# Optimization experiments

Measured on AMD Instinct MI355X. Metric: run time of the kernel, lower is better.

Reference implementation:

```python
import jax, jax.numpy as jnp
import numpy as np

D = 1024      # model_size
H = 16        # n_heads
HD = D // H   # head_size
B = 8
S = 1024


def setup_inputs() -> dict:
    key = jax.random.key(0)
    ks = jax.random.split(key, 8)
    sq = lambda k, shp: jax.random.normal(k, shp, dtype=jnp.float32) * (1.0 / np.sqrt(shp[0]))
    return {
        "query": jax.random.normal(ks[0], (B, S, D), dtype=jnp.float32),
        "value": jax.random.normal(ks[1], (B, S, D), dtype=jnp.float32),
        "Wq": sq(ks[2], (D, D)),
        "bq": jnp.zeros((D,), dtype=jnp.float32),
        "Wkv": sq(ks[3], (D, 2 * D)),
        "bkv": jnp.zeros((2 * D,), dtype=jnp.float32),
        "Wo": sq(ks[4], (D, D)),
        "bo": jnp.zeros((D,), dtype=jnp.float32),
    }


def reference(query, value, Wq, bq, Wkv, bkv, Wo, bo):
    scale = 1.0 / jnp.sqrt(jnp.float32(HD))
    q = query @ Wq + bq                      # [B,S,D]
    kv = value @ Wkv + bkv                   # [B,S,2D]
    # tf.split(kv, 2H): chunks 0..H-1 are K heads, H..2H-1 are V heads
    k = kv[..., :D].reshape(B, S, H, HD)
    v = kv[..., D:].reshape(B, S, H, HD)
    qh = q.reshape(B, S, H, HD)
    scores = jnp.einsum("bqhd,bkhd->bhqk", qh, k) * scale   # [B,H,S,S]
    attn = jax.nn.softmax(scores, axis=-1)
    heads = jnp.einsum("bhqk,bkhd->bqhd", attn, v).reshape(B, S, D)
    return heads @ Wo + bo
```

## Files before the change

### kernel.cpp

```cpp
#include <hip/hip_runtime.h>
#include <math.h>

#define B_  8
#define S_  1024
#define D_  1024
#define H_  16
#define HD_ 64

typedef float          floatx4  __attribute__((ext_vector_type(4)));
typedef __bf16         bf16x8   __attribute__((ext_vector_type(8)));
typedef unsigned int   uintx2   __attribute__((ext_vector_type(2)));
typedef unsigned int   uintx4   __attribute__((ext_vector_type(4)));

__device__ __forceinline__ unsigned short f2bf(float f) {
    union { float f; unsigned u; } v; v.f = f;
    unsigned r = v.u + 0x7FFFu + ((v.u >> 16) & 1u);
    return (unsigned short)(r >> 16);
}
__device__ __forceinline__ unsigned pk2(float a, float b) {
    union { __bf16 h[2]; unsigned u; } r;
    r.h[0] = (__bf16)a; r.h[1] = (__bf16)b;
    return r.u;
}
__device__ __forceinline__ void async16(const void* g, void* l) {
    __builtin_amdgcn_global_load_lds(
        (__attribute__((address_space(1))) void*)g,
        (__attribute__((address_space(3))) void*)l, 16, 0, 0);
}

__global__ __launch_bounds__(256) void prep_k(const float* __restrict__ query,
                                              const float* __restrict__ value,
                                              unsigned short* __restrict__ qbf,
                                              unsigned short* __restrict__ vbf,
                                              const float* __restrict__ Wq,
                                              const float* __restrict__ Wkv,
                                              const float* __restrict__ Wo,
                                              unsigned short* __restrict__ WqT,
                                              unsigned short* __restrict__ WkvT,
                                              unsigned short* __restrict__ WoT) {
    __shared__ float T[64 * 68];
    const int t   = threadIdx.x;
    const int bid = blockIdx.x;
    if (bid < 8192) {
        int i = bid * 256 + t;
        floatx4 a = ((const floatx4*)query)[i];
        floatx4 b = ((const floatx4*)value)[i];
        uintx2 oa = { pk2(a[0], a[1]), pk2(a[2], a[3]) };
        uintx2 ob = { pk2(b[0], b[1]), pk2(b[2], b[3]) };
        ((uintx2*)qbf)[i] = oa;
        ((uintx2*)vbf)[i] = ob;
        return;
    }
    const int lin = bid - 8192;
    const int z   = lin >> 8;
    const float* W; unsigned short* WT; int Ndim, nbase;
    if (z == 0)      { W = Wq;  WT = WqT;  Ndim = 1024; nbase = 0; }
    else if (z == 3) { W = Wo;  WT = WoT;  Ndim = 1024; nbase = 0; }
    else             { W = Wkv; WT = WkvT; Ndim = 2048; nbase = (z - 1) * 1024; }
    const int n0 = (lin & 15) * 64 + nbase;
    const int k0 = ((lin >> 4) & 15) * 64;
#pragma unroll
    for (int rep = 0; rep < 4; ++rep) {
        int kl = (t >> 4) + rep * 16;
        int ns = (t & 15) * 4;
        *(floatx4*)(T + kl * 68 + ns) = *(const floatx4*)(W + (size_t)(k0 + kl) * Ndim + n0 + ns);
    }
    __syncthreads();
#pragma unroll
    for (int rep = 0; rep < 2; ++rep) {
        int nl = (t >> 3) + rep * 32;
        int ks = (t & 7) * 8;
        union { unsigned short s[8]; uintx4 u; } o;
#pragma unroll
        for (int j = 0; j < 8; ++j) o.s[j] = f2bf(T[(ks + j) * 68 + nl]);
        *(uintx4*)(WT + (size_t)(n0 + nl) * 1024 + k0 + ks) = o.u;
    }
}

template<int SWAP>
__device__ __forceinline__ void kloop(const unsigned short* __restrict__ ga0,
                                      const unsigned short* __restrict__ gb0,
                                      unsigned short* __restrict__ As,
                                      unsigned short* __restrict__ Bs,
                                      floatx4 (&acc)[4][4],
                                      int w, int lane) {
    const int quad = lane >> 4;
    const int l15  = lane & 15;
    const int e7   = l15 & 7;
    const int wr   = (w >> 1) * 64;
    const int wc   = (w & 1) * 64;
    for (int k0 = 0; k0 < 1024; k0 += 64) {
        if (k0) __syncthreads();
#pragma unroll
        for (int i = 0; i < 4; ++i) {
            int c = i * 4 + w;
            async16(ga0 + (size_t)(c * 8) * 1024 + k0, As + c * 512);
            async16(gb0 + (size_t)(c * 8) * 1024 + k0, Bs + c * 512);
        }
        __syncthreads();
#pragma unroll
        for (int ks = 0; ks < 2; ++ks) {
            bf16x8 af[4], bf[4];
#pragma unroll
            for (int mi = 0; mi < 4; ++mi)
                af[mi] = *(const bf16x8*)(As + (wr + mi * 16 + l15) * 64 + (((ks * 4 + quad) ^ e7) * 8));
#pragma unroll
            for (int ni = 0; ni < 4; ++ni)
                bf[ni] = *(const bf16x8*)(Bs + (wc + ni * 16 + l15) * 64 + (((ks * 4 + quad) ^ e7) * 8));
#pragma unroll
            for (int mi = 0; mi < 4; ++mi)
#pragma unroll
                for (int ni = 0; ni < 4; ++ni)
                    acc[mi][ni] = SWAP
                        ? __builtin_amdgcn_mfma_f32_16x16x32_bf16(bf[ni], af[mi], acc[mi][ni], 0, 0, 0)
                        : __builtin_amdgcn_mfma_f32_16x16x32_bf16(af[mi], bf[ni], acc[mi][ni], 0, 0, 0);
        }
    }
}

__global__ __launch_bounds__(256, 4) void qkv_gemm_k(const unsigned short* __restrict__ qbf,
                                                     const unsigned short* __restrict__ vbf,
                                                     const unsigned short* __restrict__ WqT,
                                                     const unsigned short* __restrict__ WkvT,
                                                     const float* __restrict__ bq,
                                                     const float* __restrict__ bkv,
                                                     unsigned short* __restrict__ Qb,
                                                     unsigned short* __restrict__ Kb,
                                                     unsigned short* __restrict__ Vtg,
                                                     float cexp) {
    __shared__ unsigned short As[128 * 64];
    __shared__ unsigned short Bs[128 * 64];
    const int t    = threadIdx.x;
    const int lane = t & 63;
    const int w    = t >> 6;
    const int quad = lane >> 4;
    const int l15  = lane & 15;
    const int wr   = (w >> 1) * 64;
    const int wc   = (w & 1) * 64;
    const int lrow = lane >> 3;
    const int lswz = ((lane & 7) ^ lrow) * 8;

    const int bid = blockIdx.x;
    int m0, n0;
    const unsigned short *Ap, *Wp;
    const float* bp;
    unsigned short* outp;
    float sc;
    bool vpath = false;
    if (bid < 512) {
        m0 = (bid & 63) * 128; n0 = (bid >> 6) * 128;
        Ap = qbf; Wp = WqT; bp = bq; outp = Qb; sc = cexp;
    } else {
        int b2 = bid - 512;
        m0 = (b2 & 63) * 128; n0 = (b2 >> 6) * 128;
        Ap = vbf; Wp = WkvT; bp = bkv; outp = Kb; sc = 1.0f;
        vpath = (n0 >= 1024);
    }

    floatx4 acc[4][4] = {};
    const unsigned short* ga0 = Ap + (size_t)(m0 + lrow) * 1024 + lswz;
    const unsigned short* gb0 = Wp + (size_t)(n0 + lrow) * 1024 + lswz;

    if (!vpath) {
        kloop<1>(ga0, gb0, As, Bs, acc, w, lane);
#pragma unroll
        for (int ni = 0; ni < 4; ++ni) {
            const int nb = n0 + wc + ni * 16 + quad * 4;
            const floatx4 b4 = *(const floatx4*)(bp + nb);
#pragma unroll
            for (int mi = 0; mi < 4; ++mi) {
                const int m = m0 + wr + mi * 16 + l15;
                floatx4 v = acc[mi][ni];
                uintx2 o = { pk2((v[0] + b4[0]) * sc, (v[1] + b4[1]) * sc),
                             pk2((v[2] + b4[2]) * sc, (v[3] + b4[3]) * sc) };
                *(uintx2*)(outp + (size_t)m * 1024 + (nb & 1023)) = o;
            }
        }
    } else {
        kloop<0>(ga0, gb0, As, Bs, acc, w, lane);
        const int bb = m0 >> 10;
#pragma unroll
        for (int ni = 0; ni < 4; ++ni) {
            const int n = n0 + wc + ni * 16 + l15;
            const int c = n - 1024;
            const float bv = bp[n];
#pragma unroll
            for (int mi = 0; mi < 4; ++mi) {
                const int m = m0 + wr + mi * 16 + quad * 4;
                const int s = m & 1023;
                floatx4 v = acc[mi][ni];
                uintx2 o = { pk2(v[0] + bv, v[1] + bv), pk2(v[2] + bv, v[3] + bv) };
                *(uintx2*)(Vtg + ((size_t)(bb * 1024 + c)) * 1024 + s) = o;
            }
        }
    }
}

__global__ __launch_bounds__(256, 4) void o_gemm_k(const unsigned short* __restrict__ Hb,
                                                   const unsigned short* __restrict__ WoT,
                                                   const float* __restrict__ bo,
                                                   float* __restrict__ out) {
    __shared__ unsigned short As[128 * 64];
    __shared__ unsigned short Bs[128 * 64];
    const int t    = threadIdx.x;
    const int lane = t & 63;
    const int w    = t >> 6;
    const int quad = lane >> 4;
    const int l15  = lane & 15;
    const int wr   = (w >> 1) * 64;
    const int wc   = (w & 1) * 64;
    const int lrow = lane >> 3;
    const int lswz = ((lane & 7) ^ lrow) * 8;
    const int m0   = (blockIdx.x & 63) * 128;
    const int n0   = (blockIdx.x >> 6) * 128;

    floatx4 acc[4][4] = {};
    const unsigned short* ga0 = Hb  + (size_t)(m0 + lrow) * 1024 + lswz;
    const unsigned short* gb0 = WoT + (size_t)(n0 + lrow) * 1024 + lswz;
    kloop<1>(ga0, gb0, As, Bs, acc, w, lane);

#pragma unroll
    for (int ni = 0; ni < 4; ++ni) {
        const int nb = n0 + wc + ni * 16 + quad * 4;
        const floatx4 b4 = *(const floatx4*)(bo + nb);
#pragma unroll
        for (int mi = 0; mi < 4; ++mi) {
            const int m = m0 + wr + mi * 16 + l15;
            floatx4 v = acc[mi][ni];
            floatx4 o = { v[0] + b4[0], v[1] + b4[1], v[2] + b4[2], v[3] + b4[3] };
            *(floatx4*)(out + (size_t)m * 1024 + nb) = o;
        }
    }
}

__global__ __launch_bounds__(256) void attn_kernel(const unsigned short* __restrict__ Qb,
                                                   const unsigned short* __restrict__ Kb,
                                                   const unsigned short* __restrict__ Vtg,
                                                   unsigned short* __restrict__ Hb) {
    __shared__ unsigned short QPs[128 * 64];
    __shared__ unsigned short Ks[2][64 * 64];
    __shared__ unsigned short Vs[2][64 * 64];

    const int lin = blockIdx.x;
    const int xcd = lin & 7;
    const int grp = lin >> 3;
    const int bh  = xcd * 16 + (grp >> 3);
    const int qt  = grp & 7;
    const int b   = bh >> 4;
    const int h   = bh & 15;
    const int q0  = qt * 128;

    const int t    = threadIdx.x;
    const int lane = t & 63;
    const int w    = t >> 6;
    const int quad = lane >> 4;
    const int l15  = lane & 15;
    const int e7   = l15 & 7;
    const int lrow = lane >> 3;
    const int lswz = ((lane & 7) ^ lrow) * 8;

    {
        const unsigned short* gq = Qb + ((size_t)(b * S_ + q0)) * D_ + h * HD_;
#pragma unroll
        for (int i = 0; i < 4; ++i) {
            int r0 = (w * 4 + i) * 8;
            async16(gq + (size_t)(r0 + lrow) * D_ + lswz, QPs + r0 * 64);
        }
    }
    __syncthreads();

    bf16x8 bQ[2][2];
#pragma unroll
    for (int ks = 0; ks < 2; ++ks)
#pragma unroll
        for (int ni = 0; ni < 2; ++ni)
            bQ[ks][ni] = *(const bf16x8*)(QPs + (w * 32 + ni * 16 + l15) * 64 + ((ks * 4 + quad) ^ e7) * 8);

    const unsigned short* gkbase = Kb  + ((size_t)b * S_) * D_ + h * HD_;
    const unsigned short* gvbase = Vtg + ((size_t)(b * D_ + h * HD_)) * S_;

    float   lsum[2] = { 0.f, 0.f };
    floatx4 oacc[4][2] = {};
    unsigned short* Psw = QPs + w * (32 * 64);

#pragma unroll
    for (int j = 0; j < 2; ++j) {
        int r0 = (w * 2 + j) * 8;
        async16(gkbase + (size_t)(r0 + lrow) * D_ + lswz, &Ks[0][r0 * 64]);
        async16(gvbase + (size_t)(r0 + lrow) * S_ + lswz, &Vs[0][r0 * 64]);
    }

    for (int k0 = 0; k0 < S_; k0 += 64) {
        const int cur = (k0 >> 6) & 1;
        asm volatile("s_waitcnt vmcnt(0)\n\ts_barrier" ::: "memory");
        if (k0 + 64 < S_) {
            const int nxt = cur ^ 1;
#pragma unroll
            for (int j = 0; j < 2; ++j) {
                int r0 = (w * 2 + j) * 8;
                async16(gkbase + (size_t)(k0 + 64 + r0 + lrow) * D_ + lswz, &Ks[nxt][r0 * 64]);
                async16(gvbase + (size_t)(r0 + lrow) * S_ + (k0 + 64) + lswz, &Vs[nxt][r0 * 64]);
            }
        }

        floatx4 st[4][2] = {};
#pragma unroll
        for (int ks = 0; ks < 2; ++ks) {
            bf16x8 aK[4];
#pragma unroll
            for (int mi = 0; mi < 4; ++mi)
                aK[mi] = *(const bf16x8*)(&Ks[cur][0] + (mi * 16 + l15) * 64 + ((ks * 4 + quad) ^ e7) * 8);
#pragma unroll
            for (int mi = 0; mi < 4; ++mi)
#pragma unroll
                for (int ni = 0; ni < 2; ++ni)
                    st[mi][ni] = __builtin_amdgcn_mfma_f32_16x16x32_bf16(aK[mi], bQ[ks][ni], st[mi][ni], 0, 0, 0);
        }

#pragma unroll
        for (int ni = 0; ni < 2; ++ni) {
            float ls = 0.f;
#pragma unroll
            for (int mi = 0; mi < 4; ++mi) {
                float p0 = __builtin_amdgcn_exp2f(st[mi][ni][0]);
                float p1 = __builtin_amdgcn_exp2f(st[mi][ni][1]);
                float p2 = __builtin_amdgcn_exp2f(st[mi][ni][2]);
                float p3 = __builtin_amdgcn_exp2f(st[mi][ni][3]);
                ls += (p0 + p1) + (p2 + p3);
                uintx2 pk = { pk2(p0, p1), pk2(p2, p3) };
                *(uintx2*)(Psw + (ni * 16 + l15) * 64 +
                           (((2 * mi + (quad >> 1)) ^ e7) * 8 + (quad & 1) * 4)) = pk;
            }
            lsum[ni] += ls;
        }

#pragma unroll
        for (int ks = 0; ks < 2; ++ks) {
            bf16x8 aV[4], bP[2];
#pragma unroll
            for (int mi = 0; mi < 4; ++mi)
                aV[mi] = *(const bf16x8*)(&Vs[cur][0] + (mi * 16 + l15) * 64 + ((ks * 4 + quad) ^ e7) * 8);
#pragma unroll
            for (int ni = 0; ni < 2; ++ni)
                bP[ni] = *(const bf16x8*)(Psw + (ni * 16 + l15) * 64 + ((ks * 4 + quad) ^ e7) * 8);
#pragma unroll
            for (int mi = 0; mi < 4; ++mi)
#pragma unroll
                for (int ni = 0; ni < 2; ++ni)
                    oacc[mi][ni] = __builtin_amdgcn_mfma_f32_16x16x32_bf16(aV[mi], bP[ni], oacc[mi][ni], 0, 0, 0);
        }
    }

    float rl[2];
#pragma unroll
    for (int ni = 0; ni < 2; ++ni) {
        float l = lsum[ni];
        l += __shfl_xor(l, 16);
        l += __shfl_xor(l, 32);
        rl[ni] = 1.f / l;
    }
#pragma unroll
    for (int mi = 0; mi < 4; ++mi)
#pragma unroll
        for (int ni = 0; ni < 2; ++ni) {
            uintx2 pk = { pk2(oacc[mi][ni][0] * rl[ni], oacc[mi][ni][1] * rl[ni]),
                          pk2(oacc[mi][ni][2] * rl[ni], oacc[mi][ni][3] * rl[ni]) };
            *(uintx2*)(Psw + (ni * 16 + l15) * 64 +
                       (((2 * mi + (quad >> 1)) ^ e7) * 8 + (quad & 1) * 4)) = pk;
        }
    {
        int qrow = lane >> 1;
        int kh   = lane & 1;
        size_t obase = ((size_t)(b * S_ + q0 + w * 32 + qrow)) * D_ + h * HD_ + kh * 32;
        int e = qrow & 7;
#pragma unroll
        for (int j = 0; j < 4; ++j) {
            int chunk = kh * 4 + j;
            *(uintx4*)(Hb + obase + j * 8) =
                *(const uintx4*)(Psw + qrow * 64 + ((chunk ^ e) * 8));
        }
    }
}

extern "C" void kernel_launch(void* const* d_in, const int* in_sizes, int n_in,
                              void* d_out, int out_size, void* d_ws, size_t ws_size,
                              hipStream_t stream) {
    (void)in_sizes; (void)n_in; (void)out_size; (void)ws_size;
    const float* query = (const float*)d_in[0];
    const float* value = (const float*)d_in[1];
    const float* Wq    = (const float*)d_in[2];
    const float* bq    = (const float*)d_in[3];
    const float* Wkv   = (const float*)d_in[4];
    const float* bkv   = (const float*)d_in[5];
    const float* Wo    = (const float*)d_in[6];
    const float* bo    = (const float*)d_in[7];

    const size_t MS = (size_t)B_ * S_;
    char* p = (char*)d_ws;
    unsigned short* qbf  = (unsigned short*)p; p += MS * D_ * 2;
    unsigned short* vbf  = (unsigned short*)p; p += MS * D_ * 2;
    unsigned short* WqT  = (unsigned short*)p; p += (size_t)D_ * D_ * 2;
    unsigned short* WkvT = (unsigned short*)p; p += (size_t)2 * D_ * D_ * 2;
    unsigned short* WoT  = (unsigned short*)p; p += (size_t)D_ * D_ * 2;
    unsigned short* Qb   = (unsigned short*)p; p += MS * D_ * 2;
    unsigned short* Kb   = (unsigned short*)p; p += MS * D_ * 2;
    unsigned short* Vtg  = (unsigned short*)p; p += MS * D_ * 2;
    unsigned short* Hb   = qbf;

    const float cexp = 0.125f * 1.44269504088896341f;

    prep_k<<<9216, 256, 0, stream>>>(query, value, qbf, vbf, Wq, Wkv, Wo, WqT, WkvT, WoT);
    qkv_gemm_k<<<1536, 256, 0, stream>>>(qbf, vbf, WqT, WkvT, bq, bkv, Qb, Kb, Vtg, cexp);
    attn_kernel<<<1024, 256, 0, stream>>>(Qb, Kb, Vtg, Hb);
    o_gemm_k<<<512, 256, 0, stream>>>(Hb, WoT, bo, (float*)d_out);
}
```

Measured before the change: 266.8 us.

## Triple-buffer GEMM k-loop with 256x128 tiles and 512-thread blocks

Replaces the single-buffered GEMM k-loop with a three-stage LDS ring fed by async global-to-LDS copies, issued two tiles ahead with explicit vmcnt waits. Blocks grow to 512 threads computing 256x128 tiles, which halves the grid for the QKV and output projections. The MFMA sections get raised wave priority in both the GEMMs and the attention kernel. The aim is to hide global load latency behind matrix math and improve operand reuse, at the cost of more LDS per block (144 KB), fewer resident blocks and extra barriers.

```diff
diff --git a/kernel.cpp b/kernel.cpp
--- a/kernel.cpp
+++ b/kernel.cpp
@@ -78,35 +78,67 @@
 }
 
 template<int SWAP>
-__device__ __forceinline__ void kloop(const unsigned short* __restrict__ ga0,
-                                      const unsigned short* __restrict__ gb0,
-                                      unsigned short* __restrict__ As,
-                                      unsigned short* __restrict__ Bs,
-                                      floatx4 (&acc)[4][4],
-                                      int w, int lane) {
+__device__ __forceinline__ void kloop256(const unsigned short* __restrict__ ga0,
+                                         const unsigned short* __restrict__ gb0,
+                                         unsigned short* __restrict__ As,
+                                         unsigned short* __restrict__ Bs,
+                                         floatx4 (&acc)[4][4],
+                                         int w, int lane) {
     const int quad = lane >> 4;
     const int l15  = lane & 15;
     const int e7   = l15 & 7;
     const int wr   = (w >> 1) * 64;
     const int wc   = (w & 1) * 64;
-    for (int k0 = 0; k0 < 1024; k0 += 64) {
-        if (k0) __syncthreads();
-#pragma unroll
-        for (int i = 0; i < 4; ++i) {
-            int c = i * 4 + w;
-            async16(ga0 + (size_t)(c * 8) * 1024 + k0, As + c * 512);
-            async16(gb0 + (size_t)(c * 8) * 1024 + k0, Bs + c * 512);
-        }
-        __syncthreads();
+
+#pragma unroll
+    for (int tp = 0; tp < 2; ++tp) {
+#pragma unroll
+        for (int i = 0; i < 4; ++i)
+            async16(ga0 + (size_t)((w * 4 + i) * 8) * 1024 + tp * 64,
+                    As + tp * 16384 + (w * 4 + i) * 512);
+#pragma unroll
+        for (int j = 0; j < 2; ++j)
+            async16(gb0 + (size_t)((w * 2 + j) * 8) * 1024 + tp * 64,
+                    Bs + tp * 8192 + (w * 2 + j) * 512);
+    }
+
+    int bufc = 0, bufs = 2;
+#pragma unroll 1
+    for (int t = 0; t < 16; ++t) {
+        if (t < 15) asm volatile("s_waitcnt vmcnt(6)" ::: "memory");
+        else        asm volatile("s_waitcnt vmcnt(0)" ::: "memory");
+        __builtin_amdgcn_s_barrier();
+
+        const unsigned short* Ac  = As + bufc * 16384;
+        const unsigned short* Bc  = Bs + bufc * 8192;
+        unsigned short*       Asd = As + bufs * 16384;
+        unsigned short*       Bsd = Bs + bufs * 8192;
+        const int  k0p  = (t + 2) * 64;
+        const bool more = (t + 2) < 16;
+
 #pragma unroll
         for (int ks = 0; ks < 2; ++ks) {
             bf16x8 af[4], bf[4];
 #pragma unroll
             for (int mi = 0; mi < 4; ++mi)
-                af[mi] = *(const bf16x8*)(As + (wr + mi * 16 + l15) * 64 + (((ks * 4 + quad) ^ e7) * 8));
+                af[mi] = *(const bf16x8*)(Ac + (wr + mi * 16 + l15) * 64 + (((ks * 4 + quad) ^ e7) * 8));
 #pragma unroll
             for (int ni = 0; ni < 4; ++ni)
-                bf[ni] = *(const bf16x8*)(Bs + (wc + ni * 16 + l15) * 64 + (((ks * 4 + quad) ^ e7) * 8));
+                bf[ni] = *(const bf16x8*)(Bc + (wc + ni * 16 + l15) * 64 + (((ks * 4 + quad) ^ e7) * 8));
+            if (more) {
+                if (ks == 0) {
+                    async16(ga0 + (size_t)((w * 4 + 0) * 8) * 1024 + k0p, Asd + (w * 4 + 0) * 512);
+                    async16(ga0 + (size_t)((w * 4 + 1) * 8) * 1024 + k0p, Asd + (w * 4 + 1) * 512);
+                    async16(gb0 + (size_t)((w * 2 + 0) * 8) * 1024 + k0p, Bsd + (w * 2 + 0) * 512);
+                } else {
+                    async16(ga0 + (size_t)((w * 4 + 2) * 8) * 1024 + k0p, Asd + (w * 4 + 2) * 512);
+                    async16(ga0 + (size_t)((w * 4 + 3) * 8) * 1024 + k0p, Asd + (w * 4 + 3) * 512);
+                    async16(gb0 + (size_t)((w * 2 + 1) * 8) * 1024 + k0p, Bsd + (w * 2 + 1) * 512);
+                }
+            }
+            __builtin_amdgcn_s_barrier();
+            __builtin_amdgcn_sched_barrier(0);
+            __builtin_amdgcn_s_setprio(1);
 #pragma unroll
             for (int mi = 0; mi < 4; ++mi)
 #pragma unroll
@@ -114,11 +146,16 @@
                     acc[mi][ni] = SWAP
                         ? __builtin_amdgcn_mfma_f32_16x16x32_bf16(bf[ni], af[mi], acc[mi][ni], 0, 0, 0)
                         : __builtin_amdgcn_mfma_f32_16x16x32_bf16(af[mi], bf[ni], acc[mi][ni], 0, 0, 0);
-        }
-    }
-}
-
-__global__ __launch_bounds__(256, 4) void qkv_gemm_k(const unsigned short* __restrict__ qbf,
+            __builtin_amdgcn_s_setprio(0);
+            __builtin_amdgcn_sched_barrier(0);
+            if (ks == 0) __builtin_amdgcn_s_barrier();
+        }
+        bufc = (bufc == 2) ? 0 : bufc + 1;
+        bufs = (bufs == 2) ? 0 : bufs + 1;
+    }
+}
+
+__global__ __launch_bounds__(512, 2) void qkv_gemm_k(const unsigned short* __restrict__ qbf,
                                                      const unsigned short* __restrict__ vbf,
                                                      const unsigned short* __restrict__ WqT,
                                                      const unsigned short* __restrict__ WkvT,
@@ -128,8 +165,8 @@
                                                      unsigned short* __restrict__ Kb,
                                                      unsigned short* __restrict__ Vtg,
                                                      float cexp) {
-    __shared__ unsigned short As[128 * 64];
-    __shared__ unsigned short Bs[128 * 64];
+    __shared__ unsigned short As[3 * 16384];
+    __shared__ unsigned short Bs[3 * 8192];
     const int t    = threadIdx.x;
     const int lane = t & 63;
     const int w    = t >> 6;
@@ -147,12 +184,12 @@
     unsigned short* outp;
     float sc;
     bool vpath = false;
-    if (bid < 512) {
-        m0 = (bid & 63) * 128; n0 = (bid >> 6) * 128;
+    if (bid < 256) {
+        m0 = (bid & 31) * 256; n0 = (bid >> 5) * 128;
         Ap = qbf; Wp = WqT; bp = bq; outp = Qb; sc = cexp;
     } else {
-        int b2 = bid - 512;
-        m0 = (b2 & 63) * 128; n0 = (b2 >> 6) * 128;
+        int b2 = bid - 256;
+        m0 = (b2 & 31) * 256; n0 = (b2 >> 5) * 128;
         Ap = vbf; Wp = WkvT; bp = bkv; outp = Kb; sc = 1.0f;
         vpath = (n0 >= 1024);
     }
@@ -162,7 +199,7 @@
     const unsigned short* gb0 = Wp + (size_t)(n0 + lrow) * 1024 + lswz;
 
     if (!vpath) {
-        kloop<1>(ga0, gb0, As, Bs, acc, w, lane);
+        kloop256<1>(ga0, gb0, As, Bs, acc, w, lane);
 #pragma unroll
         for (int ni = 0; ni < 4; ++ni) {
             const int nb = n0 + wc + ni * 16 + quad * 4;
@@ -177,7 +214,7 @@
             }
         }
     } else {
-        kloop<0>(ga0, gb0, As, Bs, acc, w, lane);
+        kloop256<0>(ga0, gb0, As, Bs, acc, w, lane);
         const int bb = m0 >> 10;
 #pragma unroll
         for (int ni = 0; ni < 4; ++ni) {
@@ -196,12 +233,12 @@
     }
 }
 
-__global__ __launch_bounds__(256, 4) void o_gemm_k(const unsigned short* __restrict__ Hb,
+__global__ __launch_bounds__(512, 2) void o_gemm_k(const unsigned short* __restrict__ Hb,
                                                    const unsigned short* __restrict__ WoT,
                                                    const float* __restrict__ bo,
                                                    float* __restrict__ out) {
-    __shared__ unsigned short As[128 * 64];
-    __shared__ unsigned short Bs[128 * 64];
+    __shared__ unsigned short As[3 * 16384];
+    __shared__ unsigned short Bs[3 * 8192];
     const int t    = threadIdx.x;
     const int lane = t & 63;
     const int w    = t >> 6;
@@ -211,13 +248,13 @@
     const int wc   = (w & 1) * 64;
     const int lrow = lane >> 3;
     const int lswz = ((lane & 7) ^ lrow) * 8;
-    const int m0   = (blockIdx.x & 63) * 128;
-    const int n0   = (blockIdx.x >> 6) * 128;
+    const int m0   = (blockIdx.x & 31) * 256;
+    const int n0   = (blockIdx.x >> 5) * 128;
 
     floatx4 acc[4][4] = {};
     const unsigned short* ga0 = Hb  + (size_t)(m0 + lrow) * 1024 + lswz;
     const unsigned short* gb0 = WoT + (size_t)(n0 + lrow) * 1024 + lswz;
-    kloop<1>(ga0, gb0, As, Bs, acc, w, lane);
+    kloop256<1>(ga0, gb0, As, Bs, acc, w, lane);
 
 #pragma unroll
     for (int ni = 0; ni < 4; ++ni) {
@@ -310,11 +347,13 @@
 #pragma unroll
             for (int mi = 0; mi < 4; ++mi)
                 aK[mi] = *(const bf16x8*)(&Ks[cur][0] + (mi * 16 + l15) * 64 + ((ks * 4 + quad) ^ e7) * 8);
+            __builtin_amdgcn_s_setprio(1);
 #pragma unroll
             for (int mi = 0; mi < 4; ++mi)
 #pragma unroll
                 for (int ni = 0; ni < 2; ++ni)
                     st[mi][ni] = __builtin_amdgcn_mfma_f32_16x16x32_bf16(aK[mi], bQ[ks][ni], st[mi][ni], 0, 0, 0);
+            __builtin_amdgcn_s_setprio(0);
         }
 
 #pragma unroll
@@ -343,11 +382,13 @@
 #pragma unroll
             for (int ni = 0; ni < 2; ++ni)
                 bP[ni] = *(const bf16x8*)(Psw + (ni * 16 + l15) * 64 + ((ks * 4 + quad) ^ e7) * 8);
+            __builtin_amdgcn_s_setprio(1);
 #pragma unroll
             for (int mi = 0; mi < 4; ++mi)
 #pragma unroll
                 for (int ni = 0; ni < 2; ++ni)
                     oacc[mi][ni] = __builtin_amdgcn_mfma_f32_16x16x32_bf16(aV[mi], bP[ni], oacc[mi][ni], 0, 0, 0);
+            __builtin_amdgcn_s_setprio(0);
         }
     }
 
@@ -410,7 +451,7 @@
     const float cexp = 0.125f * 1.44269504088896341f;
 
     prep_k<<<9216, 256, 0, stream>>>(query, value, qbf, vbf, Wq, Wkv, Wo, WqT, WkvT, WoT);
-    qkv_gemm_k<<<1536, 256, 0, stream>>>(qbf, vbf, WqT, WkvT, bq, bkv, Qb, Kb, Vtg, cexp);
+    qkv_gemm_k<<<768, 512, 0, stream>>>(qbf, vbf, WqT, WkvT, bq, bkv, Qb, Kb, Vtg, cexp);
     attn_kernel<<<1024, 256, 0, stream>>>(Qb, Kb, Vtg, Hb);
-    o_gemm_k<<<512, 256, 0, stream>>>(Hb, WoT, bo, (float*)d_out);
-}
+    o_gemm_k<<<256, 512, 0, stream>>>(Hb, WoT, bo, (float*)d_out);
+}
```

Measured after the change: 269.9 us. Within noise of the previous version (+1.2%).

## Software-pipeline attention loop: prefetch K two tiles ahead and overlap next QK^T

Applied to the files above, without the earlier changes.

Restructures the flash-attention inner loop so the QK^T MFMAs for tile k+1 are issued between the softmax exp of tile k and its PV MFMAs. K is now staged two tiles ahead and V one tile ahead, with ping-pong score register sets unrolled by two. It also wraps the MFMA blocks in s_setprio to favour matrix issue across waves. This aims to hide exp latency and LDS/global load latency behind matrix work, at the cost of more registers (two score sets), which may lower occupancy.

```diff
diff --git a/kernel.cpp b/kernel.cpp
--- a/kernel.cpp
+++ b/kernel.cpp
@@ -283,49 +283,64 @@
     floatx4 oacc[4][2] = {};
     unsigned short* Psw = QPs + w * (32 * 64);
 
-#pragma unroll
-    for (int j = 0; j < 2; ++j) {
-        int r0 = (w * 2 + j) * 8;
-        async16(gkbase + (size_t)(r0 + lrow) * D_ + lswz, &Ks[0][r0 * 64]);
-        async16(gvbase + (size_t)(r0 + lrow) * S_ + lswz, &Vs[0][r0 * 64]);
-    }
-
-    for (int k0 = 0; k0 < S_; k0 += 64) {
-        const int cur = (k0 >> 6) & 1;
-        asm volatile("s_waitcnt vmcnt(0)\n\ts_barrier" ::: "memory");
-        if (k0 + 64 < S_) {
-            const int nxt = cur ^ 1;
-#pragma unroll
-            for (int j = 0; j < 2; ++j) {
-                int r0 = (w * 2 + j) * 8;
-                async16(gkbase + (size_t)(k0 + 64 + r0 + lrow) * D_ + lswz, &Ks[nxt][r0 * 64]);
-                async16(gvbase + (size_t)(r0 + lrow) * S_ + (k0 + 64) + lswz, &Vs[nxt][r0 * 64]);
-            }
-        }
-
-        floatx4 st[4][2] = {};
+    auto stageK = [&](int kt, int buf) {
+#pragma unroll
+        for (int j = 0; j < 2; ++j) {
+            int r0 = (w * 2 + j) * 8;
+            async16(gkbase + (size_t)(kt * 64 + r0 + lrow) * D_ + lswz, &Ks[buf][r0 * 64]);
+        }
+    };
+    auto stageV = [&](int kt, int buf) {
+#pragma unroll
+        for (int j = 0; j < 2; ++j) {
+            int r0 = (w * 2 + j) * 8;
+            async16(gvbase + (size_t)(r0 + lrow) * S_ + kt * 64 + lswz, &Vs[buf][r0 * 64]);
+        }
+    };
+    auto qk = [&](int buf, floatx4 (&st)[4][2]) {
+#pragma unroll
+        for (int mi = 0; mi < 4; ++mi)
+#pragma unroll
+            for (int ni = 0; ni < 2; ++ni)
+                st[mi][ni] = floatx4{0.f, 0.f, 0.f, 0.f};
 #pragma unroll
         for (int ks = 0; ks < 2; ++ks) {
             bf16x8 aK[4];
 #pragma unroll
             for (int mi = 0; mi < 4; ++mi)
-                aK[mi] = *(const bf16x8*)(&Ks[cur][0] + (mi * 16 + l15) * 64 + ((ks * 4 + quad) ^ e7) * 8);
+                aK[mi] = *(const bf16x8*)(&Ks[buf][0] + (mi * 16 + l15) * 64 + ((ks * 4 + quad) ^ e7) * 8);
+            __builtin_amdgcn_s_setprio(1);
 #pragma unroll
             for (int mi = 0; mi < 4; ++mi)
 #pragma unroll
                 for (int ni = 0; ni < 2; ++ni)
                     st[mi][ni] = __builtin_amdgcn_mfma_f32_16x16x32_bf16(aK[mi], bQ[ks][ni], st[mi][ni], 0, 0, 0);
-        }
+            __builtin_amdgcn_s_setprio(0);
+        }
+    };
+
+    stageK(0, 0);
+    stageK(1, 1);
+    stageV(0, 0);
+    asm volatile("s_waitcnt vmcnt(4)\n\ts_barrier" ::: "memory");
+
+    floatx4 stA[4][2], stB[4][2];
+    qk(0, stA);
+
+    auto body = [&](int kt, floatx4 (&stC)[4][2], floatx4 (&stN)[4][2]) {
+        asm volatile("s_waitcnt vmcnt(0)\n\ts_barrier" ::: "memory");
+        if (kt < 14) stageK(kt + 2, kt & 1);
+        if (kt < 15) stageV(kt + 1, (kt + 1) & 1);
 
 #pragma unroll
         for (int ni = 0; ni < 2; ++ni) {
             float ls = 0.f;
 #pragma unroll
             for (int mi = 0; mi < 4; ++mi) {
-                float p0 = __builtin_amdgcn_exp2f(st[mi][ni][0]);
-                float p1 = __builtin_amdgcn_exp2f(st[mi][ni][1]);
-                float p2 = __builtin_amdgcn_exp2f(st[mi][ni][2]);
-                float p3 = __builtin_amdgcn_exp2f(st[mi][ni][3]);
+                float p0 = __builtin_amdgcn_exp2f(stC[mi][ni][0]);
+                float p1 = __builtin_amdgcn_exp2f(stC[mi][ni][1]);
+                float p2 = __builtin_amdgcn_exp2f(stC[mi][ni][2]);
+                float p3 = __builtin_amdgcn_exp2f(stC[mi][ni][3]);
                 ls += (p0 + p1) + (p2 + p3);
                 uintx2 pk = { pk2(p0, p1), pk2(p2, p3) };
                 *(uintx2*)(Psw + (ni * 16 + l15) * 64 +
@@ -334,21 +349,31 @@
             lsum[ni] += ls;
         }
 
+        if (kt < 15) qk((kt + 1) & 1, stN);
+
 #pragma unroll
         for (int ks = 0; ks < 2; ++ks) {
             bf16x8 aV[4], bP[2];
 #pragma unroll
             for (int mi = 0; mi < 4; ++mi)
-                aV[mi] = *(const bf16x8*)(&Vs[cur][0] + (mi * 16 + l15) * 64 + ((ks * 4 + quad) ^ e7) * 8);
+                aV[mi] = *(const bf16x8*)(&Vs[kt & 1][0] + (mi * 16 + l15) * 64 + ((ks * 4 + quad) ^ e7) * 8);
 #pragma unroll
             for (int ni = 0; ni < 2; ++ni)
                 bP[ni] = *(const bf16x8*)(Psw + (ni * 16 + l15) * 64 + ((ks * 4 + quad) ^ e7) * 8);
+            __builtin_amdgcn_s_setprio(1);
 #pragma unroll
             for (int mi = 0; mi < 4; ++mi)
 #pragma unroll
                 for (int ni = 0; ni < 2; ++ni)
                     oacc[mi][ni] = __builtin_amdgcn_mfma_f32_16x16x32_bf16(aV[mi], bP[ni], oacc[mi][ni], 0, 0, 0);
-        }
+            __builtin_amdgcn_s_setprio(0);
+        }
+    };
+
+#pragma unroll 1
+    for (int it = 0; it < 8; ++it) {
+        body(2 * it,     stA, stB);
+        body(2 * it + 1, stB, stA);
     }
 
     float rl[2];
```

Result: no change. 268.7 us (+0.7%).
